# Kernel optimization log

Measured on AMD Instinct MI355X. Metric: run time of the kernel, lower is better.

Reference implementation:

```python
import jax, jax.numpy as jnp
import numpy as np

EPS = 1e-5          # InstanceNorm eps (torch default)
KERNEL = 25         # moving_avg_kernel_size
TAU = 1.0           # gumbel softmax temperature
REGIME_NUM = 8


def _inorm(x):
    # InstanceNorm1d without affine on (N, C, L): normalize over last dim (biased var)
    m = x.mean(-1, keepdims=True)
    v = ((x - m) ** 2).mean(-1, keepdims=True)
    return (x - m) * jax.lax.rsqrt(v + EPS)


def _lbr(x, W, b):
    # Linear -> InstanceNorm (over last dim) -> exact GELU
    return jax.nn.gelu(_inorm(x @ W + b), approximate=False)


def _moving_avg(x, k):
    # x: (B, L, C); edge-replicate pad (k-1)//2 on both sides, sliding mean via cumsum
    p = (k - 1) // 2
    xp = jnp.concatenate([jnp.repeat(x[:, :1], p, axis=1), x,
                          jnp.repeat(x[:, -1:], p, axis=1)], axis=1)
    cs = jnp.concatenate([jnp.zeros_like(xp[:, :1]), jnp.cumsum(xp, axis=1)], axis=1)
    return (cs[:, k:] - cs[:, :-k]) / k  # (B, L, C)


def _encode(x, Ws, bs, Wt, bt):
    # inputs - inputs[:, 0:1]; series decomposition; seasonal+trend branches
    x = x - x[:, :1]
    mm = _moving_avg(x, KERNEL)
    return _lbr(x - mm, Ws, bs) + _lbr(mm, Wt, bt)  # (B, L, H)


def reference(inputs_longterm, inputs_shortterm,
              Ws, bs, Wt, bt,
              Wh1, bh1, Wl1, bl1, Wh2, bh2, Wl2, bl2, Wh3, bh3, Wl3, bl3,
              Wr, br, proto):
    e_lt = _encode(inputs_longterm, Ws, bs, Wt, bt)   # (B, L_lt, H)
    e_st = _encode(inputs_shortterm, Ws, bs, Wt, bt)  # (B, L_st, H)

    # RegimeEncoder: alternate hidden-dim and lookback-dim LinearBatchRelu layers
    o = _lbr(e_lt, Wh1, bh1)
    o = jnp.swapaxes(_lbr(jnp.swapaxes(o, 1, 2), Wl1, bl1), 1, 2)
    o = _lbr(o, Wh2, bh2)
    o = jnp.swapaxes(_lbr(jnp.swapaxes(o, 1, 2), Wl2, bl2), 1, 2)
    o = _lbr(o, Wh3, bh3)
    o = jnp.swapaxes(_lbr(jnp.swapaxes(o, 1, 2), Wl3, bl3), 1, 2)  # (B, L_lt//8, H)
    logits = o.reshape(o.shape[0], -1) @ Wr + br  # (B, R)

    # gumbel_softmax(hard=True) with straight-through estimator
    g = jax.random.gumbel(jax.random.key(42), logits.shape, logits.dtype)
    y_soft = jax.nn.softmax((logits + g) / TAU, axis=-1)
    y_hard = jax.nn.one_hot(jnp.argmax(y_soft, axis=-1), REGIME_NUM, dtype=logits.dtype)
    w = y_hard - jax.lax.stop_gradient(y_soft) + y_soft  # (B, R)

    # weighted sum over regime prototypes, then combine with encoded shortterm
    sel = jnp.einsum('br,rnhmo->bnhmo', w, proto)          # (B, L_st, H, M, 3)
    out = jnp.einsum('bnh,bnhmo->bmo', e_st, sel)          # (B, M, 3)
    B = out.shape[0]
    return jax.nn.softmax(out.reshape(B, -1), axis=-1).reshape(out.shape)


def setup_inputs() -> dict:
    key = jax.random.key(0)
    ks = jax.random.split(key, 24)
    B, L_lt, L_st, C, H, R, M = 32, 512, 128, 9, 128, 8, 64
    s = 0.02
    d = {
        'inputs_longterm':  jax.random.normal(ks[0], (B, L_lt, C), jnp.float32),
        'inputs_shortterm': jax.random.normal(ks[1], (B, L_st, C), jnp.float32),
        'Ws': jax.random.normal(ks[2], (C, H), jnp.float32) * s,
        'bs': jnp.zeros((H,), jnp.float32),
        'Wt': jax.random.normal(ks[3], (C, H), jnp.float32) * s,
        'bt': jnp.zeros((H,), jnp.float32),
        'Wh1': jax.random.normal(ks[4], (H, H), jnp.float32) * s,
        'bh1': jnp.zeros((H,), jnp.float32),
        'Wl1': jax.random.normal(ks[5], (L_lt, L_lt // 2), jnp.float32) * s,
        'bl1': jnp.zeros((L_lt // 2,), jnp.float32),
        'Wh2': jax.random.normal(ks[6], (H, H), jnp.float32) * s,
        'bh2': jnp.zeros((H,), jnp.float32),
        'Wl2': jax.random.normal(ks[7], (L_lt // 2, L_lt // 4), jnp.float32) * s,
        'bl2': jnp.zeros((L_lt // 4,), jnp.float32),
        'Wh3': jax.random.normal(ks[8], (H, H), jnp.float32) * s,
        'bh3': jnp.zeros((H,), jnp.float32),
        'Wl3': jax.random.normal(ks[9], (L_lt // 4, L_lt // 8), jnp.float32) * s,
        'bl3': jnp.zeros((L_lt // 8,), jnp.float32),
        'Wr': jax.random.normal(ks[10], (H * L_lt // 8, R), jnp.float32) * s,
        'br': jnp.zeros((R,), jnp.float32),
        'proto': jax.random.normal(ks[11], (R, L_st, H, M, 3), jnp.float32),
    }
    return d
```

## Files before the change

### kernel.cpp

```cpp
#include <hip/hip_runtime.h>
#include <math.h>

#define EPS 1e-5f

__device__ __forceinline__ float gelu_exact(float x) {
    return 0.5f * x * (1.0f + erff(x * 0.7071067811865476f));
}

__device__ float block_sum(float v, float* red) {
    int lane = threadIdx.x & 63, wid = threadIdx.x >> 6;
#pragma unroll
    for (int off = 32; off > 0; off >>= 1) v += __shfl_down(v, off, 64);
    if (lane == 0) red[wid] = v;
    __syncthreads();
    int nw = ((int)blockDim.x + 63) >> 6;
    float s = red[0];
    for (int w = 1; w < nw; w++) s += red[w];
    __syncthreads();
    return s;
}

__device__ float block_max(float v, float* red) {
    int lane = threadIdx.x & 63, wid = threadIdx.x >> 6;
#pragma unroll
    for (int off = 32; off > 0; off >>= 1) v = fmaxf(v, __shfl_down(v, off, 64));
    if (lane == 0) red[wid] = v;
    __syncthreads();
    int nw = ((int)blockDim.x + 63) >> 6;
    float s = red[0];
    for (int w = 1; w < nw; w++) s = fmaxf(s, red[w]);
    __syncthreads();
    return s;
}

__device__ void threefry2x32(unsigned k0, unsigned k1, unsigned x0, unsigned x1,
                             unsigned& o0, unsigned& o1) {
    unsigned ks[3] = {k0, k1, k0 ^ k1 ^ 0x1BD11BDAu};
    const unsigned rot[2][4] = {{13u, 15u, 26u, 6u}, {17u, 29u, 16u, 24u}};
    x0 += ks[0]; x1 += ks[1];
#pragma unroll
    for (int i = 0; i < 5; i++) {
#pragma unroll
        for (int j = 0; j < 4; j++) {
            unsigned r = rot[i & 1][j];
            x0 += x1;
            x1 = (x1 << r) | (x1 >> (32 - r));
            x1 ^= x0;
        }
        x0 += ks[(i + 1) % 3];
        x1 += ks[(i + 2) % 3] + (unsigned)(i + 1);
    }
    o0 = x0; o1 = x1;
}

__device__ float gumbel_at(int j) {
    unsigned o0, o1;
    threefry2x32(0u, 42u, 0u, (unsigned)j, o0, o1);
    unsigned bits = o0 ^ o1;
    float f = __uint_as_float((bits >> 9) | 0x3F800000u) - 1.0f;
    float u = fmaxf(f + 1.17549435e-38f, 1.17549435e-38f);
    return -logf(-logf(u));
}

__global__ __launch_bounds__(256) void encode_kernel(
    const float* __restrict__ x_lt, const float* __restrict__ x_st,
    const float* __restrict__ Ws, const float* __restrict__ bs,
    const float* __restrict__ Wt, const float* __restrict__ bt,
    float* __restrict__ e_lt, float* __restrict__ e_st) {
    const int b = blockIdx.y;
    const int w = threadIdx.x >> 6, ln = threadIdx.x & 63;
    const float* x; float* e; int L, l;
    if (blockIdx.x < 128) { x = x_lt; e = e_lt; L = 512; l = blockIdx.x * 4 + w; }
    else { x = x_st; e = e_st; L = 128; l = (blockIdx.x - 128) * 4 + w; }
    __shared__ float xw_all[4][228];
    __shared__ float sm_all[4][20];
    float* xw = xw_all[w];
    float* sm = sm_all[w];
    const float* xb = x + (size_t)b * L * 9;
#pragma unroll
    for (int q = 0; q < 4; q++) {
        int f = ln + 64 * q;
        if (f < 225) {
            int row = f / 9, c = f - row * 9;
            int rr = l - 12 + row;
            rr = rr < 0 ? 0 : (rr >= L ? L - 1 : rr);
            xw[f] = xb[(size_t)rr * 9 + c];
        }
    }
    __syncthreads();
    if (ln < 9) {
        float s = 0.f;
#pragma unroll
        for (int j = 0; j < 25; j++) s += xw[j * 9 + ln];
        float x0 = xb[ln];
        float mm = (s - 25.f * x0) * (1.0f / 25.0f);
        sm[ln] = (xw[108 + ln] - x0) - mm;
        sm[ln + 10] = mm;
    }
    __syncthreads();
    float ysA = bs[ln], ysB = bs[ln + 64];
    float ytA = bt[ln], ytB = bt[ln + 64];
#pragma unroll
    for (int c = 0; c < 9; c++) {
        float sv = sm[c], mv = sm[c + 10];
        ysA += sv * Ws[c * 128 + ln];
        ysB += sv * Ws[c * 128 + ln + 64];
        ytA += mv * Wt[c * 128 + ln];
        ytB += mv * Wt[c * 128 + ln + 64];
    }
    float sa = ysA + ysB, sb2 = ytA + ytB;
#pragma unroll
    for (int off = 32; off > 0; off >>= 1) {
        sa += __shfl_xor(sa, off, 64);
        sb2 += __shfl_xor(sb2, off, 64);
    }
    float ms = sa * (1.0f / 128.0f), mt = sb2 * (1.0f / 128.0f);
    float dA = ysA - ms, dB = ysB - ms;
    float tA = ytA - mt, tB = ytB - mt;
    float qa = dA * dA + dB * dB, qb = tA * tA + tB * tB;
#pragma unroll
    for (int off = 32; off > 0; off >>= 1) {
        qa += __shfl_xor(qa, off, 64);
        qb += __shfl_xor(qb, off, 64);
    }
    float inva = rsqrtf(qa * (1.0f / 128.0f) + EPS);
    float invb = rsqrtf(qb * (1.0f / 128.0f) + EPS);
    float* eo = e + ((size_t)b * L + l) * 128;
    eo[ln] = gelu_exact(dA * inva) + gelu_exact(tA * invb);
    eo[ln + 64] = gelu_exact(dB * inva) + gelu_exact(tB * invb);
}

template <int K, int N, int WR, bool TRANS>
__global__ __launch_bounds__(256) void lbr_wave(
    const float* __restrict__ A, int S, int ABOFF,
    const float* __restrict__ W, const float* __restrict__ bias,
    float* __restrict__ out, int OROWS, int OBOFF) {
    constexpr int CG = N / 4;
    constexpr int SG = 64 / CG;
    constexpr int RW = SG * WR;
    constexpr int MT = 4 * RW;
    constexpr int LOG2MT = (MT == 8) ? 3 : ((MT == 16) ? 4 : 5);
    constexpr int STAGE = 4 * RW * K;
    constexpr int TILE = TRANS ? MT * (N + 4) : 0;
    constexpr int LSZ = STAGE > TILE ? STAGE : TILE;
    __shared__ __align__(16) float lds[LSZ];
    const int t = threadIdx.x;
    const int w = t >> 6, ln = t & 63;
    const int sg = ln / CG;
    const int n0 = (ln % CG) * 4;
    const int b = blockIdx.y;
    const int r0b = blockIdx.x * MT;
    const int r0w = r0b + w * RW;
    float* As = lds + w * RW * K;
    const float* Ab = A + (size_t)b * ABOFF;
    for (int idx = ln; idx < RW * (K / 4); idx += 64) {
        int rr = idx / (K / 4), kk = idx % (K / 4);
        float4 v = *(const float4*)(Ab + (size_t)(r0w + rr) * S + kk * 4);
        *(float4*)(As + rr * K + kk * 4) = v;
    }
    float4 acc[WR];
    {
        float4 bv = *(const float4*)(bias + n0);
#pragma unroll
        for (int j = 0; j < WR; j++) acc[j] = bv;
    }
    const float* ap = As + (sg * WR) * K;
    const float* wp = W + n0;
#pragma unroll 2
    for (int k = 0; k < K; k += 4) {
        float4 w0 = *(const float4*)(wp);
        float4 w1 = *(const float4*)(wp + N);
        float4 w2 = *(const float4*)(wp + 2 * N);
        float4 w3 = *(const float4*)(wp + 3 * N);
        wp += 4 * N;
#pragma unroll
        for (int j = 0; j < WR; j++) {
            float4 a4 = *(const float4*)(ap + j * K + k);
            acc[j].x += a4.x * w0.x; acc[j].y += a4.x * w0.y;
            acc[j].z += a4.x * w0.z; acc[j].w += a4.x * w0.w;
            acc[j].x += a4.y * w1.x; acc[j].y += a4.y * w1.y;
            acc[j].z += a4.y * w1.z; acc[j].w += a4.y * w1.w;
            acc[j].x += a4.z * w2.x; acc[j].y += a4.z * w2.y;
            acc[j].z += a4.z * w2.z; acc[j].w += a4.z * w2.w;
            acc[j].x += a4.w * w3.x; acc[j].y += a4.w * w3.y;
            acc[j].z += a4.w * w3.z; acc[j].w += a4.w * w3.w;
        }
    }
    float4 res[WR];
#pragma unroll
    for (int j = 0; j < WR; j++) {
        float s = acc[j].x + acc[j].y + acc[j].z + acc[j].w;
#pragma unroll
        for (int off = CG / 2; off > 0; off >>= 1) s += __shfl_xor(s, off, 64);
        float m = s * (1.0f / (float)N);
        float dx = acc[j].x - m, dy = acc[j].y - m, dz = acc[j].z - m, dw = acc[j].w - m;
        float q = dx * dx + dy * dy + dz * dz + dw * dw;
#pragma unroll
        for (int off = CG / 2; off > 0; off >>= 1) q += __shfl_xor(q, off, 64);
        float inv = rsqrtf(q * (1.0f / (float)N) + EPS);
        res[j].x = gelu_exact(dx * inv);
        res[j].y = gelu_exact(dy * inv);
        res[j].z = gelu_exact(dz * inv);
        res[j].w = gelu_exact(dw * inv);
    }
    if constexpr (TRANS) {
        __syncthreads();
#pragma unroll
        for (int j = 0; j < WR; j++) {
            int rl = w * RW + sg * WR + j;
            *(float4*)(lds + rl * (N + 4) + n0) = res[j];
        }
        __syncthreads();
        float* ob = out + (size_t)b * OBOFF + r0b;
        for (int e = t; e < MT * N; e += 256) {
            int r = e & (MT - 1), n = e >> LOG2MT;
            ob[(size_t)n * OROWS + r] = lds[r * (N + 4) + n];
        }
    } else {
        float* ob = out + (size_t)b * OBOFF;
#pragma unroll
        for (int j = 0; j < WR; j++) {
            int row = r0w + sg * WR + j;
            *(float4*)(ob + (size_t)row * N + n0) = res[j];
        }
    }
}

__global__ __launch_bounds__(256) void logits_select(
    const float* __restrict__ O6, const float* __restrict__ Wr,
    const float* __restrict__ br, float* __restrict__ sel_w, int* __restrict__ sel_r) {
    int b = blockIdx.x, t = threadIdx.x;
    __shared__ float sO6[128 * 68];
    __shared__ float red[4][8];
    const float4* ob4 = (const float4*)(O6 + (size_t)b * 8192);
    for (int i4 = t; i4 < 2048; i4 += 256) {
        float4 v = ob4[i4];
        int p = i4 * 4;
        int h = p >> 6, l4 = p & 63;
        *(float4*)(&sO6[h * 68 + l4]) = v;
    }
    __syncthreads();
    float acc[8] = {0, 0, 0, 0, 0, 0, 0, 0};
#pragma unroll 4
    for (int q = 0; q < 32; q++) {
        int i = q * 256 + t;
        int l4 = i >> 7, h = i & 127;
        float v = sO6[h * 68 + l4];
        const float4* wr = (const float4*)(Wr + (size_t)i * 8);
        float4 w0 = wr[0], w1 = wr[1];
        acc[0] += v * w0.x; acc[1] += v * w0.y; acc[2] += v * w0.z; acc[3] += v * w0.w;
        acc[4] += v * w1.x; acc[5] += v * w1.y; acc[6] += v * w1.z; acc[7] += v * w1.w;
    }
#pragma unroll
    for (int j = 0; j < 8; j++)
#pragma unroll
        for (int off = 32; off > 0; off >>= 1) acc[j] += __shfl_xor(acc[j], off, 64);
    int lane = t & 63, wid = t >> 6;
    if (lane == 0)
        for (int j = 0; j < 8; j++) red[wid][j] = acc[j];
    __syncthreads();
    if (t == 0) {
        float z[8];
        for (int j = 0; j < 8; j++) {
            float lg = br[j] + red[0][j] + red[1][j] + red[2][j] + red[3][j];
            z[j] = lg + gumbel_at(b * 8 + j);
        }
        int am = 0;
        float zm = z[0];
        for (int j = 1; j < 8; j++)
            if (z[j] > zm) { zm = z[j]; am = j; }
        float ssum = 0.f;
        for (int j = 0; j < 8; j++) ssum += expf(z[j] - zm);
        float s = 1.0f / ssum;
        sel_w[b] = (1.0f - s) + s;
        sel_r[b] = am;
    }
}

__global__ __launch_bounds__(192) void einsum_nsplit(
    const float* __restrict__ e_st, const float* __restrict__ proto,
    const int* __restrict__ sel_r, float* __restrict__ part) {
    const int n = blockIdx.x, r = blockIdx.y, hz = blockIdx.z, t = threadIdx.x;
    __shared__ int loc[32];
    __shared__ int s_gs;
    if (t == 0) {
        int g = 0;
        for (int bb = 0; bb < 32; bb++)
            if (sel_r[bb] == r) loc[g++] = bb;
        s_gs = g;
    }
    __syncthreads();
    const int gs = s_gs;
    if (gs == 0) return;
    __shared__ __align__(16) float es[8][64];
    const float* pb = proto + (((size_t)r * 128 + n) * 128 + hz * 64) * 192 + t;
    float* po = part + (size_t)hz * (32 * 128 * 192);
    for (int s0 = 0; s0 < gs; s0 += 8) {
        int np = gs - s0 < 8 ? gs - s0 : 8;
        __syncthreads();
        for (int i = t; i < 512; i += 192) {
            int sb = i >> 6, h = i & 63;
            float v = 0.f;
            if (sb < np)
                v = e_st[((size_t)loc[s0 + sb] * 128 + n) * 128 + hz * 64 + h];
            es[sb][h] = v;
        }
        __syncthreads();
        float a[8] = {0, 0, 0, 0, 0, 0, 0, 0};
#pragma unroll
        for (int h = 0; h < 64; h += 8) {
            float p[8];
#pragma unroll
            for (int u = 0; u < 8; u++) p[u] = pb[(size_t)(h + u) * 192];
#pragma unroll
            for (int sb = 0; sb < 8; sb++) {
                float4 e0 = *(const float4*)(&es[sb][h]);
                float4 e1 = *(const float4*)(&es[sb][h + 4]);
                a[sb] += e0.x * p[0] + e0.y * p[1] + e0.z * p[2] + e0.w * p[3]
                       + e1.x * p[4] + e1.y * p[5] + e1.z * p[6] + e1.w * p[7];
            }
        }
#pragma unroll
        for (int sb = 0; sb < 8; sb++) {
            if (sb < np) {
                int bb = loc[s0 + sb];
                po[((size_t)bb * 128 + n) * 192 + t] = a[sb];
            }
        }
    }
}

__global__ void finalize_kernel(const float* __restrict__ part, const float* __restrict__ sel_w,
                                float* __restrict__ out) {
    int b = blockIdx.x, t = threadIdx.x;
    __shared__ float red[4];
    const float* p0 = part + (size_t)b * 128 * 192 + t;
    const float* p1 = p0 + (size_t)32 * 128 * 192;
    float v = 0.f;
#pragma unroll 8
    for (int c = 0; c < 128; c++) {
        v += p0[(size_t)c * 192];
        v += p1[(size_t)c * 192];
    }
    v *= sel_w[b];
    float mx = block_max(v, red);
    float e = expf(v - mx);
    float s = block_sum(e, red);
    out[(size_t)b * 192 + t] = e / s;
}

extern "C" void kernel_launch(void* const* d_in, const int* in_sizes, int n_in,
                              void* d_out, int out_size, void* d_ws, size_t ws_size,
                              hipStream_t stream) {
    const float* in_lt = (const float*)d_in[0];
    const float* in_st = (const float*)d_in[1];
    const float* Ws  = (const float*)d_in[2];  const float* bs  = (const float*)d_in[3];
    const float* Wt  = (const float*)d_in[4];  const float* bt  = (const float*)d_in[5];
    const float* Wh1 = (const float*)d_in[6];  const float* bh1 = (const float*)d_in[7];
    const float* Wl1 = (const float*)d_in[8];  const float* bl1 = (const float*)d_in[9];
    const float* Wh2 = (const float*)d_in[10]; const float* bh2 = (const float*)d_in[11];
    const float* Wl2 = (const float*)d_in[12]; const float* bl2 = (const float*)d_in[13];
    const float* Wh3 = (const float*)d_in[14]; const float* bh3 = (const float*)d_in[15];
    const float* Wl3 = (const float*)d_in[16]; const float* bl3 = (const float*)d_in[17];
    const float* Wr  = (const float*)d_in[18]; const float* br  = (const float*)d_in[19];
    const float* proto = (const float*)d_in[20];
    float* out = (float*)d_out;

    float* ws = (float*)d_ws;
    size_t off = 0;
    float* e_lt = ws + off; off += (size_t)32 * 512 * 128;
    float* e_st = ws + off; off += (size_t)32 * 128 * 128;
    float* O1T = ws + off; off += (size_t)128 * 16384;
    float* O2T = ws + off; off += (size_t)256 * 4096;
    float* O3T = ws + off; off += (size_t)128 * 8192;
    float* O4T = ws + off; off += (size_t)128 * 4096;
    float* O5T = ws + off; off += (size_t)128 * 4096;
    float* O6 = ws + off; off += (size_t)32 * 128 * 64;
    float* part = ws + off; off += (size_t)2 * 32 * 128 * 192;
    float* sel_w = ws + off; off += 32;
    int* sel_r = (int*)(ws + off); off += 32;

    encode_kernel<<<dim3(160, 32), 256, 0, stream>>>(in_lt, in_st, Ws, bs, Wt, bt, e_lt, e_st);
    lbr_wave<128, 128, 4, true><<<dim3(512, 1), 256, 0, stream>>>(
        e_lt, 128, 0, Wh1, bh1, O1T, 16384, 0);
    lbr_wave<512, 256, 2, true><<<dim3(16, 32), 256, 0, stream>>>(
        O1T, 16384, 512, Wl1, bl1, O2T, 4096, 128);
    lbr_wave<128, 128, 2, true><<<dim3(16, 32), 256, 0, stream>>>(
        O2T, 4096, 128, Wh2, bh2, O3T, 8192, 256);
    lbr_wave<256, 128, 1, true><<<dim3(16, 32), 256, 0, stream>>>(
        O3T, 8192, 256, Wl2, bl2, O4T, 4096, 128);
    lbr_wave<128, 128, 1, true><<<dim3(16, 32), 256, 0, stream>>>(
        O4T, 4096, 128, Wh3, bh3, O5T, 4096, 128);
    lbr_wave<128, 64, 1, false><<<dim3(8, 32), 256, 0, stream>>>(
        O5T, 4096, 128, Wl3, bl3, O6, 0, 8192);
    logits_select<<<32, 256, 0, stream>>>(O6, Wr, br, sel_w, sel_r);
    einsum_nsplit<<<dim3(128, 8, 2), 192, 0, stream>>>(e_st, proto, sel_r, part);
    finalize_kernel<<<32, 192, 0, stream>>>(part, sel_w, out);
}
```

Measured before the change: 371.7 us.

## Vectorize proto loads in einsum with float4 and split h across lane groups

Restructures the einsum kernel so each thread loads float4 chunks of the prototype tensor covering four output columns, with four lane groups per wavefront each handling a quarter of the h rows. Partial sums are combined with cross-lane shuffles and written back as float4 by the first 16 lanes. The shared e_st tile is transposed so each row's eight batch values are read with two float4 loads. The goal is wider, fewer global loads on the bandwidth-bound proto stream. The cost is extra shuffle reductions, more accumulator registers, and a launch-bounds occupancy hint.

```diff
diff --git a/kernel.cpp b/kernel.cpp
--- a/kernel.cpp
+++ b/kernel.cpp
@@ -277,10 +277,13 @@
     }
 }
 
-__global__ __launch_bounds__(192) void einsum_nsplit(
+__global__ __launch_bounds__(192, 4) void einsum_nsplit(
     const float* __restrict__ e_st, const float* __restrict__ proto,
     const int* __restrict__ sel_r, float* __restrict__ part) {
     const int n = blockIdx.x, r = blockIdx.y, hz = blockIdx.z, t = threadIdx.x;
+    const int w = t >> 6, ln = t & 63;
+    const int rg = ln >> 4;
+    const int q4 = (w * 16 + (ln & 15)) * 4;
     __shared__ int loc[32];
     __shared__ int s_gs;
     if (t == 0) {
@@ -292,8 +295,8 @@
     __syncthreads();
     const int gs = s_gs;
     if (gs == 0) return;
-    __shared__ __align__(16) float es[8][64];
-    const float* pb = proto + (((size_t)r * 128 + n) * 128 + hz * 64) * 192 + t;
+    __shared__ __align__(16) float es[64][12];
+    const float* pb = proto + (((size_t)r * 128 + n) * 128 + hz * 64) * 192;
     float* po = part + (size_t)hz * (32 * 128 * 192);
     for (int s0 = 0; s0 < gs; s0 += 8) {
         int np = gs - s0 < 8 ? gs - s0 : 8;
@@ -303,28 +306,42 @@
             float v = 0.f;
             if (sb < np)
                 v = e_st[((size_t)loc[s0 + sb] * 128 + n) * 128 + hz * 64 + h];
-            es[sb][h] = v;
+            es[h][sb] = v;
         }
         __syncthreads();
-        float a[8] = {0, 0, 0, 0, 0, 0, 0, 0};
-#pragma unroll
-        for (int h = 0; h < 64; h += 8) {
-            float p[8];
-#pragma unroll
-            for (int u = 0; u < 8; u++) p[u] = pb[(size_t)(h + u) * 192];
+        float4 a[8];
+#pragma unroll
+        for (int sb = 0; sb < 8; sb++) a[sb] = make_float4(0.f, 0.f, 0.f, 0.f);
+#pragma unroll 4
+        for (int hh = 0; hh < 16; hh++) {
+            int row = hh * 4 + rg;
+            float4 pv = *(const float4*)(pb + (size_t)row * 192 + q4);
+            float4 e0 = *(const float4*)(&es[row][0]);
+            float4 e1 = *(const float4*)(&es[row][4]);
+#define ACC4(j, s) a[j].x += (s) * pv.x; a[j].y += (s) * pv.y; \
+                   a[j].z += (s) * pv.z; a[j].w += (s) * pv.w;
+            ACC4(0, e0.x) ACC4(1, e0.y) ACC4(2, e0.z) ACC4(3, e0.w)
+            ACC4(4, e1.x) ACC4(5, e1.y) ACC4(6, e1.z) ACC4(7, e1.w)
+#undef ACC4
+        }
+#pragma unroll
+        for (int sb = 0; sb < 8; sb++) {
+            a[sb].x += __shfl_xor(a[sb].x, 16, 64);
+            a[sb].y += __shfl_xor(a[sb].y, 16, 64);
+            a[sb].z += __shfl_xor(a[sb].z, 16, 64);
+            a[sb].w += __shfl_xor(a[sb].w, 16, 64);
+            a[sb].x += __shfl_xor(a[sb].x, 32, 64);
+            a[sb].y += __shfl_xor(a[sb].y, 32, 64);
+            a[sb].z += __shfl_xor(a[sb].z, 32, 64);
+            a[sb].w += __shfl_xor(a[sb].w, 32, 64);
+        }
+        if (ln < 16) {
 #pragma unroll
             for (int sb = 0; sb < 8; sb++) {
-                float4 e0 = *(const float4*)(&es[sb][h]);
-                float4 e1 = *(const float4*)(&es[sb][h + 4]);
-                a[sb] += e0.x * p[0] + e0.y * p[1] + e0.z * p[2] + e0.w * p[3]
-                       + e1.x * p[4] + e1.y * p[5] + e1.z * p[6] + e1.w * p[7];
-            }
-        }
-#pragma unroll
-        for (int sb = 0; sb < 8; sb++) {
-            if (sb < np) {
-                int bb = loc[s0 + sb];
-                po[((size_t)bb * 128 + n) * 192 + t] = a[sb];
+                if (sb < np) {
+                    int bb = loc[s0 + sb];
+                    *(float4*)(po + ((size_t)bb * 128 + n) * 192 + q4) = a[sb];
+                }
             }
         }
     }
```

New measurement: 359.1 us. -3.4%, faster.
